# Kernel optimization log

Measured on AMD Instinct MI355X. Metric: run time of the kernel, lower is better.

Reference implementation:

```python
import jax, jax.numpy as jnp
import numpy as np

B, TQ, TK = 8, 256, 256
DQ, DK, DV, H = 512, 512, 512, 256


def setup_inputs() -> dict:
    key = jax.random.key(0)
    k1, k2, k3, k4, k5, k6 = jax.random.split(key, 6)
    queries = jax.random.normal(k1, (B, TQ, DQ), dtype=jnp.float32)
    keys = jax.random.normal(k2, (B, TK, DK), dtype=jnp.float32)
    values = jax.random.normal(k3, (B, TK, DV), dtype=jnp.float32)
    # Linear(in, out, bias=False): y = x @ W.T with W (out,in); store transposed (in,out)
    Wq = jax.random.normal(k4, (DQ, H), dtype=jnp.float32) / np.sqrt(DQ)
    Wk = jax.random.normal(k5, (DK, H), dtype=jnp.float32) / np.sqrt(DK)
    wv = jax.random.normal(k6, (H,), dtype=jnp.float32) / np.sqrt(H)
    return {"queries": queries, "keys": keys, "values": values,
            "Wq": Wq, "Wk": Wk, "wv": wv}


def reference(queries, keys, values, Wq, Wk, wv):
    q = jnp.einsum('bqd,dh->bqh', queries, Wq)          # (B,Tq,H)
    k = jnp.einsum('bkd,dh->bkh', keys, Wk)             # (B,Tk,H)
    features = jnp.tanh(q[:, :, None, :] + k[:, None, :, :])  # (B,Tq,Tk,H)
    scores = jnp.einsum('bqkh,h->bqk', features, wv)    # (B,Tq,Tk)
    attn = jax.nn.softmax(scores, axis=-1)              # (B,Tq,Tk)
    return jnp.einsum('bqk,bkv->bqv', attn, values)     # (B,Tq,Dv)
```

## Files before the change

kernel.cpp:

```cpp
#include <hip/hip_runtime.h>

typedef float v2f __attribute__((ext_vector_type(2)));
typedef short bf16x8 __attribute__((ext_vector_type(8)));
typedef float f32x4 __attribute__((ext_vector_type(4)));

namespace {
constexpr int B   = 8;
constexpr int TQ  = 256;
constexpr int TK  = 256;
constexpr int DQK = 512;
constexpr int DV  = 512;
constexpr int H   = 256;
constexpr int QB  = 4;
constexpr float C2LOG2E   = 2.8853900817779268f;
constexpr float NEG2LOG2E = -2.8853900817779268f;
}

__device__ __forceinline__ uint32_t f2u(float x) { return __builtin_bit_cast(uint32_t, x); }
__device__ __forceinline__ float u2f(uint32_t x) { return __builtin_bit_cast(float, x); }
__device__ __forceinline__ uint32_t pack_hi(float x, float y) {
    return (f2u(y) & 0xFFFF0000u) | (f2u(x) >> 16);
}

__global__ __launch_bounds__(256)
void proj_kernel(const float* __restrict__ Q, const float* __restrict__ Kin,
                 const float* __restrict__ Wq, const float* __restrict__ Wk,
                 float* __restrict__ qpc, float* __restrict__ kpc4)
{
    __shared__ short Ahi[4][64][8];
    __shared__ short Alo[4][64][8];
    __shared__ short Bhi[4][32][8];
    __shared__ short Blo[4][32][8];

    const bool kside = (blockIdx.z == 1);
    const float* A = kside ? Kin : Q;
    const float* W = kside ? Wk  : Wq;
    const int m0 = blockIdx.x * 64;
    const int n0 = blockIdx.y * 32;
    const int tid = threadIdx.x;

    const int am = tid >> 2, ag = tid & 3;
    const int bk = tid >> 3, bn4 = (tid & 7) * 4;
    const float4* aptr = (const float4*)(A + (m0 + am) * DQK) + ag * 2;
    const float*  wptr = W + bk * H + n0 + bn4;

    const int w = tid >> 6, l = tid & 63;
    const int wm = (w >> 1) * 32, wn = (w & 1) * 16;
    const int fg = l >> 4;
    const int fr = l & 15;

    float4 a0 = aptr[0], a1 = aptr[1];
    float4 bv = *(const float4*)wptr;

    f32x4 acc0 = {0.f, 0.f, 0.f, 0.f};
    f32x4 acc1 = {0.f, 0.f, 0.f, 0.f};

    for (int s = 0; s < 16; ++s) {
        __syncthreads();
        {
            float ah0 = u2f(f2u(a0.x) & 0xFFFF0000u), ah1 = u2f(f2u(a0.y) & 0xFFFF0000u);
            float ah2 = u2f(f2u(a0.z) & 0xFFFF0000u), ah3 = u2f(f2u(a0.w) & 0xFFFF0000u);
            float ah4 = u2f(f2u(a1.x) & 0xFFFF0000u), ah5 = u2f(f2u(a1.y) & 0xFFFF0000u);
            float ah6 = u2f(f2u(a1.z) & 0xFFFF0000u), ah7 = u2f(f2u(a1.w) & 0xFFFF0000u);
            int4 hw, lw;
            hw.x = (int)pack_hi(a0.x, a0.y); hw.y = (int)pack_hi(a0.z, a0.w);
            hw.z = (int)pack_hi(a1.x, a1.y); hw.w = (int)pack_hi(a1.z, a1.w);
            lw.x = (int)pack_hi(a0.x - ah0, a0.y - ah1);
            lw.y = (int)pack_hi(a0.z - ah2, a0.w - ah3);
            lw.z = (int)pack_hi(a1.x - ah4, a1.y - ah5);
            lw.w = (int)pack_hi(a1.z - ah6, a1.w - ah7);
            *(int4*)&Ahi[ag][am][0] = hw;
            *(int4*)&Alo[ag][am][0] = lw;
            const int g = bk >> 3, slot = bk & 7;
            float bb[4] = {bv.x, bv.y, bv.z, bv.w};
            #pragma unroll
            for (int i = 0; i < 4; ++i) {
                uint32_t u = f2u(bb[i]);
                float hf = u2f(u & 0xFFFF0000u);
                Bhi[g][bn4 + i][slot] = (short)(u >> 16);
                Blo[g][bn4 + i][slot] = (short)(f2u(bb[i] - hf) >> 16);
            }
        }
        __syncthreads();
        if (s < 15) {
            a0 = aptr[s * 8 + 8];
            a1 = aptr[s * 8 + 9];
            bv = *(const float4*)(wptr + (s + 1) * 32 * H);
        }
        bf16x8 ah_0 = *(const bf16x8*)&Ahi[fg][wm + fr][0];
        bf16x8 ah_1 = *(const bf16x8*)&Ahi[fg][wm + 16 + fr][0];
        bf16x8 al_0 = *(const bf16x8*)&Alo[fg][wm + fr][0];
        bf16x8 al_1 = *(const bf16x8*)&Alo[fg][wm + 16 + fr][0];
        bf16x8 bh   = *(const bf16x8*)&Bhi[fg][wn + fr][0];
        bf16x8 bl   = *(const bf16x8*)&Blo[fg][wn + fr][0];
        acc0 = __builtin_amdgcn_mfma_f32_16x16x32_bf16(ah_0, bh, acc0, 0, 0, 0);
        acc1 = __builtin_amdgcn_mfma_f32_16x16x32_bf16(ah_1, bh, acc1, 0, 0, 0);
        acc0 = __builtin_amdgcn_mfma_f32_16x16x32_bf16(ah_0, bl, acc0, 0, 0, 0);
        acc1 = __builtin_amdgcn_mfma_f32_16x16x32_bf16(ah_1, bl, acc1, 0, 0, 0);
        acc0 = __builtin_amdgcn_mfma_f32_16x16x32_bf16(al_0, bh, acc0, 0, 0, 0);
        acc1 = __builtin_amdgcn_mfma_f32_16x16x32_bf16(al_1, bh, acc1, 0, 0, 0);
    }

    const int col = n0 + wn + fr;
    #pragma unroll
    for (int mi = 0; mi < 2; ++mi) {
        f32x4 acc = mi ? acc1 : acc0;
        #pragma unroll
        for (int r = 0; r < 4; ++r) {
            const int row = m0 + wm + mi * 16 + fg * 4 + r;
            float val = __builtin_amdgcn_exp2f(acc[r] * C2LOG2E);
            if (!kside) {
                qpc[row * H + col] = val;
            } else {
                const int bb2 = row >> 8, kk = row & 255;
                kpc4[((bb2 * (H / 4) + (col >> 2)) * TK + kk) * 4 + (col & 3)] = val;
            }
        }
    }
}

__global__ __launch_bounds__(512)
void attn_kernel(const float* __restrict__ qpc, const float* __restrict__ kpc4,
                 const float* __restrict__ wv, const float* __restrict__ values,
                 float* __restrict__ out)
{
    __shared__ float qlds[H][QB];
    __shared__ float wlds[H];
    __shared__ float elds[QB][TK];
    __shared__ float rowsum[QB];
    __shared__ float accbuf[4][QB][TK];

    const int b   = blockIdx.x >> 6;
    const int q0  = (blockIdx.x & 63) * QB;
    const int tid = threadIdx.x;

    for (int i = tid; i < QB * H; i += 512) {
        const int h = i >> 2, q = i & 3;
        qlds[h][q] = qpc[(b * TQ + q0 + q) * H + h];
    }
    if (tid < H) wlds[tid] = wv[tid];
    __syncthreads();

    {
        const int kp = tid & 127;
        const int hg = tid >> 7;
        const int h0 = hg * 64;
        const float4* kc = (const float4*)kpc4 + (b * (H / 4) + (h0 >> 2)) * TK + 2 * kp;
        v2f a01a = {0.f, 0.f}, a23a = {0.f, 0.f};
        v2f a01b = {0.f, 0.f}, a23b = {0.f, 0.f};
        #pragma unroll 4
        for (int h4 = 0; h4 < 16; ++h4) {
            float4 kva4 = kc[h4 * TK];
            float4 kvb4 = kc[h4 * TK + 1];
            float4 w4 = *(const float4*)&wlds[h0 + h4 * 4];
            #pragma unroll
            for (int j = 0; j < 4; ++j) {
                const int h = h0 + h4 * 4 + j;
                const float ea = (j == 0) ? kva4.x : (j == 1) ? kva4.y : (j == 2) ? kva4.z : kva4.w;
                const float eb = (j == 0) ? kvb4.x : (j == 1) ? kvb4.y : (j == 2) ? kvb4.z : kvb4.w;
                const float wj = (j == 0) ? w4.x  : (j == 1) ? w4.y  : (j == 2) ? w4.z  : w4.w;
                float4 qa = *(const float4*)&qlds[h][0];
                v2f q01 = {qa.x, qa.y}, q23 = {qa.z, qa.w};
                v2f ea2 = {ea, ea}, eb2 = {eb, eb}, w2 = {wj, wj};
                v2f one = {1.0f, 1.0f};
                v2f d0a = __builtin_elementwise_fma(q01, ea2, one);
                v2f d1a = __builtin_elementwise_fma(q23, ea2, one);
                v2f d0b = __builtin_elementwise_fma(q01, eb2, one);
                v2f d1b = __builtin_elementwise_fma(q23, eb2, one);
                v2f r0a, r1a, r0b, r1b;
                r0a.x = __builtin_amdgcn_rcpf(d0a.x);
                r0a.y = __builtin_amdgcn_rcpf(d0a.y);
                r1a.x = __builtin_amdgcn_rcpf(d1a.x);
                r1a.y = __builtin_amdgcn_rcpf(d1a.y);
                r0b.x = __builtin_amdgcn_rcpf(d0b.x);
                r0b.y = __builtin_amdgcn_rcpf(d0b.y);
                r1b.x = __builtin_amdgcn_rcpf(d1b.x);
                r1b.y = __builtin_amdgcn_rcpf(d1b.y);
                a01a = __builtin_elementwise_fma(w2, r0a, a01a);
                a23a = __builtin_elementwise_fma(w2, r1a, a23a);
                a01b = __builtin_elementwise_fma(w2, r0b, a01b);
                a23b = __builtin_elementwise_fma(w2, r1b, a23b);
            }
        }
        accbuf[hg][0][2 * kp]     = a01a.x;
        accbuf[hg][1][2 * kp]     = a01a.y;
        accbuf[hg][2][2 * kp]     = a23a.x;
        accbuf[hg][3][2 * kp]     = a23a.y;
        accbuf[hg][0][2 * kp + 1] = a01b.x;
        accbuf[hg][1][2 * kp + 1] = a01b.y;
        accbuf[hg][2][2 * kp + 1] = a23b.x;
        accbuf[hg][3][2 * kp + 1] = a23b.y;
    }
    __syncthreads();

    for (int i = tid; i < QB * TK; i += 512) {
        const int q = i >> 8, kk = i & 255;
        float s = (accbuf[0][q][kk] + accbuf[1][q][kk]) +
                  (accbuf[2][q][kk] + accbuf[3][q][kk]);
        elds[q][kk] = __builtin_amdgcn_exp2f(s * NEG2LOG2E);
    }
    __syncthreads();

    {
        const int q = (tid >> 6) & 3, lane = tid & 63;
        float4 v = *(const float4*)&elds[q][lane * 4];
        float s = (v.x + v.y) + (v.z + v.w);
        #pragma unroll
        for (int off = 1; off < 64; off <<= 1)
            s += __shfl_xor(s, off);
        if (tid < 256 && lane == 0) rowsum[q] = s;
    }
    __syncthreads();

    {
        const int c = tid & 255, kh = tid >> 8;
        const float* vb = values + (b * TK + kh * 128) * DV;
        float* pvout = &accbuf[0][0][0];
        v2f o[QB] = {};
        for (int kk = 0; kk < 128; ++kk) {
            v2f vv = {vb[kk * DV + c], vb[kk * DV + c + 256]};
            const int kc = kh * 128 + kk;
            #pragma unroll
            for (int q = 0; q < QB; ++q) {
                float e = elds[q][kc];
                v2f e2 = {e, e};
                o[q] = __builtin_elementwise_fma(e2, vv, o[q]);
            }
        }
        #pragma unroll
        for (int q = 0; q < QB; ++q) {
            pvout[(kh * QB + q) * DV + c]       = o[q].x;
            pvout[(kh * QB + q) * DV + c + 256] = o[q].y;
        }
    }
    __syncthreads();

    {
        const float* pvout = &accbuf[0][0][0];
        for (int i = tid; i < QB * DV; i += 512) {
            const int q = i >> 9, c = i & 511;
            float val = (pvout[q * DV + c] + pvout[(QB + q) * DV + c]) *
                        __builtin_amdgcn_rcpf(rowsum[q]);
            out[(b * TQ + q0 + q) * DV + c] = val;
        }
    }
}

extern "C" void kernel_launch(void* const* d_in, const int* in_sizes, int n_in,
                              void* d_out, int out_size, void* d_ws, size_t ws_size,
                              hipStream_t stream)
{
    const float* queries = (const float*)d_in[0];
    const float* keys    = (const float*)d_in[1];
    const float* values  = (const float*)d_in[2];
    const float* Wq      = (const float*)d_in[3];
    const float* Wk      = (const float*)d_in[4];
    const float* wv      = (const float*)d_in[5];
    float* out  = (float*)d_out;
    float* qpc  = (float*)d_ws;
    float* kpc4 = qpc + B * TQ * H;

    dim3 gproj(B * TQ / 64, H / 32, 2);
    proj_kernel<<<gproj, 256, 0, stream>>>(queries, keys, Wq, Wk, qpc, kpc4);
    attn_kernel<<<B * (TQ / QB), 512, 0, stream>>>(qpc, kpc4, wv, values, out);
}
```

Baseline: 46.67 us.

## Split attention into score and PV kernels with larger query tile for PV

```diff
diff --git a/kernel.cpp b/kernel.cpp
--- a/kernel.cpp
+++ b/kernel.cpp
@@ -12,6 +12,7 @@
 constexpr int DV  = 512;
 constexpr int H   = 256;
 constexpr int QB  = 4;
+constexpr int PVQ = 8;
 constexpr float C2LOG2E   = 2.8853900817779268f;
 constexpr float NEG2LOG2E = -2.8853900817779268f;
 }
@@ -120,14 +121,13 @@
 }
 
 __global__ __launch_bounds__(512)
-void attn_kernel(const float* __restrict__ qpc, const float* __restrict__ kpc4,
-                 const float* __restrict__ wv, const float* __restrict__ values,
-                 float* __restrict__ out)
+void score_kernel(const float* __restrict__ qpc, const float* __restrict__ kpc4,
+                  const float* __restrict__ wv, float* __restrict__ p_out,
+                  float* __restrict__ rowsum_g)
 {
     __shared__ float qlds[H][QB];
     __shared__ float wlds[H];
     __shared__ float elds[QB][TK];
-    __shared__ float rowsum[QB];
     __shared__ float accbuf[4][QB][TK];
 
     const int b   = blockIdx.x >> 6;
@@ -152,13 +152,12 @@
         for (int h4 = 0; h4 < 16; ++h4) {
             float4 kva4 = kc[h4 * TK];
             float4 kvb4 = kc[h4 * TK + 1];
-            float4 w4 = *(const float4*)&wlds[h0 + h4 * 4];
             #pragma unroll
             for (int j = 0; j < 4; ++j) {
                 const int h = h0 + h4 * 4 + j;
                 const float ea = (j == 0) ? kva4.x : (j == 1) ? kva4.y : (j == 2) ? kva4.z : kva4.w;
                 const float eb = (j == 0) ? kvb4.x : (j == 1) ? kvb4.y : (j == 2) ? kvb4.z : kvb4.w;
-                const float wj = (j == 0) ? w4.x  : (j == 1) ? w4.y  : (j == 2) ? w4.z  : w4.w;
+                const float wj = wlds[h];
                 float4 qa = *(const float4*)&qlds[h][0];
                 v2f q01 = {qa.x, qa.y}, q23 = {qa.z, qa.w};
                 v2f ea2 = {ea, ea}, eb2 = {eb, eb}, w2 = {wj, wj};
@@ -197,7 +196,9 @@
         const int q = i >> 8, kk = i & 255;
         float s = (accbuf[0][q][kk] + accbuf[1][q][kk]) +
                   (accbuf[2][q][kk] + accbuf[3][q][kk]);
-        elds[q][kk] = __builtin_amdgcn_exp2f(s * NEG2LOG2E);
+        float e = __builtin_amdgcn_exp2f(s * NEG2LOG2E);
+        elds[q][kk] = e;
+        p_out[(b * TQ + q0 + q) * TK + kk] = e;
     }
     __syncthreads();
 
@@ -208,42 +209,38 @@
         #pragma unroll
         for (int off = 1; off < 64; off <<= 1)
             s += __shfl_xor(s, off);
-        if (tid < 256 && lane == 0) rowsum[q] = s;
-    }
-    __syncthreads();
-
-    {
-        const int c = tid & 255, kh = tid >> 8;
-        const float* vb = values + (b * TK + kh * 128) * DV;
-        float* pvout = &accbuf[0][0][0];
-        v2f o[QB] = {};
-        for (int kk = 0; kk < 128; ++kk) {
-            v2f vv = {vb[kk * DV + c], vb[kk * DV + c + 256]};
-            const int kc = kh * 128 + kk;
-            #pragma unroll
-            for (int q = 0; q < QB; ++q) {
-                float e = elds[q][kc];
-                v2f e2 = {e, e};
-                o[q] = __builtin_elementwise_fma(e2, vv, o[q]);
-            }
-        }
+        if (tid < 256 && lane == 0) rowsum_g[b * TQ + q0 + q] = s;
+    }
+}
+
+__global__ __launch_bounds__(512)
+void pv_kernel(const float* __restrict__ p, const float* __restrict__ rowsum_g,
+               const float* __restrict__ values, float* __restrict__ out)
+{
+    __shared__ float plds[PVQ][TK];
+    __shared__ float rs[PVQ];
+
+    const int b   = blockIdx.x >> 5;
+    const int q0  = (blockIdx.x & 31) * PVQ;
+    const int tid = threadIdx.x;
+
+    for (int i = tid; i < PVQ * TK; i += 512)
+        plds[i >> 8][i & 255] = p[(b * TQ + q0 + (i >> 8)) * TK + (i & 255)];
+    if (tid < PVQ) rs[tid] = rowsum_g[b * TQ + q0 + tid];
+    __syncthreads();
+
+    const float* vb = values + b * TK * DV + tid;
+    float o[PVQ] = {};
+    #pragma unroll 4
+    for (int kk = 0; kk < TK; ++kk) {
+        float v = vb[kk * DV];
         #pragma unroll
-        for (int q = 0; q < QB; ++q) {
-            pvout[(kh * QB + q) * DV + c]       = o[q].x;
-            pvout[(kh * QB + q) * DV + c + 256] = o[q].y;
-        }
-    }
-    __syncthreads();
-
-    {
-        const float* pvout = &accbuf[0][0][0];
-        for (int i = tid; i < QB * DV; i += 512) {
-            const int q = i >> 9, c = i & 511;
-            float val = (pvout[q * DV + c] + pvout[(QB + q) * DV + c]) *
-                        __builtin_amdgcn_rcpf(rowsum[q]);
-            out[(b * TQ + q0 + q) * DV + c] = val;
-        }
-    }
+        for (int q = 0; q < PVQ; ++q)
+            o[q] = fmaf(plds[q][kk], v, o[q]);
+    }
+    #pragma unroll
+    for (int q = 0; q < PVQ; ++q)
+        out[(b * TQ + q0 + q) * DV + tid] = o[q] * __builtin_amdgcn_rcpf(rs[q]);
 }
 
 extern "C" void kernel_launch(void* const* d_in, const int* in_sizes, int n_in,
@@ -256,11 +253,14 @@
     const float* Wq      = (const float*)d_in[3];
     const float* Wk      = (const float*)d_in[4];
     const float* wv      = (const float*)d_in[5];
-    float* out  = (float*)d_out;
-    float* qpc  = (float*)d_ws;
-    float* kpc4 = qpc + B * TQ * H;
+    float* out    = (float*)d_out;
+    float* qpc    = (float*)d_ws;
+    float* kpc4   = qpc + B * TQ * H;
+    float* p_ws   = kpc4 + B * H * TK;
+    float* rs_ws  = p_ws + B * TQ * TK;
 
     dim3 gproj(B * TQ / 64, H / 32, 2);
     proj_kernel<<<gproj, 256, 0, stream>>>(queries, keys, Wq, Wk, qpc, kpc4);
-    attn_kernel<<<B * (TQ / QB), 512, 0, stream>>>(qpc, kpc4, wv, values, out);
-}
+    score_kernel<<<B * (TQ / QB), 512, 0, stream>>>(qpc, kpc4, wv, p_ws, rs_ws);
+    pv_kernel<<<B * (TQ / PVQ), 512, 0, stream>>>(p_ws, rs_ws, values, out);
+}
```

After: 58.43 us. 25.2% more time.

## Fuse rowsum into exp pass and restructure PV loop over full key range

Applied to the files above, without the earlier changes.

```diff
diff --git a/kernel.cpp b/kernel.cpp
--- a/kernel.cpp
+++ b/kernel.cpp
@@ -126,9 +126,9 @@
 {
     __shared__ float qlds[H][QB];
     __shared__ float wlds[H];
-    __shared__ float elds[QB][TK];
+    __shared__ float accbuf[4][QB][TK];
+    __shared__ float pT[TK][QB];
     __shared__ float rowsum[QB];
-    __shared__ float accbuf[4][QB][TK];
 
     const int b   = blockIdx.x >> 6;
     const int q0  = (blockIdx.x & 63) * QB;
@@ -139,6 +139,7 @@
         qlds[h][q] = qpc[(b * TQ + q0 + q) * H + h];
     }
     if (tid < H) wlds[tid] = wv[tid];
+    if (tid < QB) rowsum[tid] = 0.0f;
     __syncthreads();
 
     {
@@ -152,13 +153,12 @@
         for (int h4 = 0; h4 < 16; ++h4) {
             float4 kva4 = kc[h4 * TK];
             float4 kvb4 = kc[h4 * TK + 1];
-            float4 w4 = *(const float4*)&wlds[h0 + h4 * 4];
             #pragma unroll
             for (int j = 0; j < 4; ++j) {
                 const int h = h0 + h4 * 4 + j;
                 const float ea = (j == 0) ? kva4.x : (j == 1) ? kva4.y : (j == 2) ? kva4.z : kva4.w;
                 const float eb = (j == 0) ? kvb4.x : (j == 1) ? kvb4.y : (j == 2) ? kvb4.z : kvb4.w;
-                const float wj = (j == 0) ? w4.x  : (j == 1) ? w4.y  : (j == 2) ? w4.z  : w4.w;
+                const float wj = wlds[h];
                 float4 qa = *(const float4*)&qlds[h][0];
                 v2f q01 = {qa.x, qa.y}, q23 = {qa.z, qa.w};
                 v2f ea2 = {ea, ea}, eb2 = {eb, eb}, w2 = {wj, wj};
@@ -194,55 +194,38 @@
     __syncthreads();
 
     for (int i = tid; i < QB * TK; i += 512) {
-        const int q = i >> 8, kk = i & 255;
+        const int kk = i >> 2, q = i & 3;
         float s = (accbuf[0][q][kk] + accbuf[1][q][kk]) +
                   (accbuf[2][q][kk] + accbuf[3][q][kk]);
-        elds[q][kk] = __builtin_amdgcn_exp2f(s * NEG2LOG2E);
+        float e = __builtin_amdgcn_exp2f(s * NEG2LOG2E);
+        pT[kk][q] = e;
+        float r = e;
+        r += __shfl_xor(r, 4);
+        r += __shfl_xor(r, 8);
+        r += __shfl_xor(r, 16);
+        r += __shfl_xor(r, 32);
+        if ((tid & 63) < 4) atomicAdd(&rowsum[tid & 63], r);
     }
     __syncthreads();
 
     {
-        const int q = (tid >> 6) & 3, lane = tid & 63;
-        float4 v = *(const float4*)&elds[q][lane * 4];
-        float s = (v.x + v.y) + (v.z + v.w);
-        #pragma unroll
-        for (int off = 1; off < 64; off <<= 1)
-            s += __shfl_xor(s, off);
-        if (tid < 256 && lane == 0) rowsum[q] = s;
-    }
-    __syncthreads();
-
-    {
-        const int c = tid & 255, kh = tid >> 8;
-        const float* vb = values + (b * TK + kh * 128) * DV;
-        float* pvout = &accbuf[0][0][0];
-        v2f o[QB] = {};
-        for (int kk = 0; kk < 128; ++kk) {
-            v2f vv = {vb[kk * DV + c], vb[kk * DV + c + 256]};
-            const int kc = kh * 128 + kk;
-            #pragma unroll
-            for (int q = 0; q < QB; ++q) {
-                float e = elds[q][kc];
-                v2f e2 = {e, e};
-                o[q] = __builtin_elementwise_fma(e2, vv, o[q]);
-            }
-        }
-        #pragma unroll
-        for (int q = 0; q < QB; ++q) {
-            pvout[(kh * QB + q) * DV + c]       = o[q].x;
-            pvout[(kh * QB + q) * DV + c + 256] = o[q].y;
-        }
-    }
-    __syncthreads();
-
-    {
-        const float* pvout = &accbuf[0][0][0];
-        for (int i = tid; i < QB * DV; i += 512) {
-            const int q = i >> 9, c = i & 511;
-            float val = (pvout[q * DV + c] + pvout[(QB + q) * DV + c]) *
-                        __builtin_amdgcn_rcpf(rowsum[q]);
-            out[(b * TQ + q0 + q) * DV + c] = val;
-        }
+        const int c = tid;
+        const float* vb = values + b * TK * DV + c;
+        float o0 = 0.f, o1 = 0.f, o2 = 0.f, o3 = 0.f;
+        #pragma unroll 4
+        for (int kk = 0; kk < TK; ++kk) {
+            float v = vb[kk * DV];
+            float4 p4 = *(const float4*)&pT[kk][0];
+            o0 = fmaf(p4.x, v, o0);
+            o1 = fmaf(p4.y, v, o1);
+            o2 = fmaf(p4.z, v, o2);
+            o3 = fmaf(p4.w, v, o3);
+        }
+        float* ob = out + (b * TQ + q0) * DV + c;
+        ob[0 * DV] = o0 * __builtin_amdgcn_rcpf(rowsum[0]);
+        ob[1 * DV] = o1 * __builtin_amdgcn_rcpf(rowsum[1]);
+        ob[2 * DV] = o2 * __builtin_amdgcn_rcpf(rowsum[2]);
+        ob[3 * DV] = o3 * __builtin_amdgcn_rcpf(rowsum[3]);
     }
 }
 
```

Measured after the change: 56.83 us. 21.8% more time.
